# Kernel tuning notes

Hardware: AMD Instinct MI355X
Metric: run time of the kernel (lower is better)

The kernel has to match this reference:

```python
import jax, jax.numpy as jnp
import numpy as np

N_NODES = 50000
N_EDGES = 800000
IN_FEATS, H_FEATS, OUT_FEATS = 64, 128, 64
NUM_RELS = 2


def setup_inputs() -> dict:
    key = jax.random.key(0)
    ks = jax.random.split(key, 10)
    s = 0.05
    return {
        "feat": jax.random.normal(ks[0], (N_NODES, IN_FEATS), dtype=jnp.float32),
        "W1": jax.random.normal(ks[1], (NUM_RELS, IN_FEATS, H_FEATS), dtype=jnp.float32) * s,
        "loop1": jax.random.normal(ks[2], (IN_FEATS, H_FEATS), dtype=jnp.float32) * s,
        "b1": jnp.zeros((H_FEATS,), dtype=jnp.float32),
        "W2": jax.random.normal(ks[3], (NUM_RELS, H_FEATS, OUT_FEATS), dtype=jnp.float32) * s,
        "loop2": jax.random.normal(ks[4], (H_FEATS, OUT_FEATS), dtype=jnp.float32) * s,
        "b2": jnp.zeros((OUT_FEATS,), dtype=jnp.float32),
        "src": jax.random.randint(ks[5], (N_EDGES,), 0, N_NODES, dtype=jnp.int32),
        "dst": jax.random.randint(ks[6], (N_EDGES,), 0, N_NODES, dtype=jnp.int32),
        "etype": jax.random.randint(ks[7], (N_EDGES,), 0, NUM_RELS, dtype=jnp.int32),
    }


def _rel_graph_conv(x, W, loop_w, b, src, dst, etype, n_nodes):
    # Per-relation transform at node granularity (cheaper than per-edge W gather
    # since E >> N), then per-edge select by relation, gather by src,
    # scatter-sum into dst. Matches DGL RelGraphConv (regularizer=None,
    # self_loop=True, bias=True, sum aggregation).
    x0 = x @ W[0]  # [N, out]
    x1 = x @ W[1]  # [N, out]
    msg = jnp.where((etype == 0)[:, None], x0[src], x1[src])  # [E, out]
    agg = jax.ops.segment_sum(msg, dst, num_segments=n_nodes)  # [N, out]
    return agg + x @ loop_w + b


def reference(feat, W1, loop1, b1, W2, loop2, b2, src, dst, etype):
    n = feat.shape[0]
    h = _rel_graph_conv(feat, W1, loop1, b1, src, dst, etype, n)
    h = jax.nn.relu(h)
    h = _rel_graph_conv(h, W2, loop2, b2, src, dst, etype, n)
    return h
```

## Files before the change

kernel.cpp:

```cpp
#include <hip/hip_runtime.h>
#include <hip/hip_bf16.h>


#define N_IN   64
#define N_HID  128
#define N_OUT  64

typedef __attribute__((ext_vector_type(8))) short  bf16x8;
typedef __attribute__((ext_vector_type(4))) float  f32x4;

__device__ __forceinline__ ushort f2bf(float f) {
    uint u = __float_as_uint(f);
    u += 0x7FFFu + ((u >> 16) & 1u);
    return (ushort)(u >> 16);
}
__device__ __forceinline__ float bf2f(ushort h) {
    return __uint_as_float(((uint)h) << 16);
}
__device__ __forceinline__ float bfu_lo(uint u) { return __uint_as_float(u << 16); }
__device__ __forceinline__ float bfu_hi(uint u) { return __uint_as_float(u & 0xFFFF0000u); }

__global__ void hist_kernel(const int* __restrict__ dst, int* __restrict__ cnt, int E) {
    for (int e = blockIdx.x * blockDim.x + threadIdx.x; e < E;
         e += gridDim.x * blockDim.x)
        atomicAdd(&cnt[dst[e]], 1);
}

__global__ void scan_reduce_kernel(const int* __restrict__ cnt, int* __restrict__ bsum, int N) {
    __shared__ int s[1024];
    int i = blockIdx.x * 1024 + threadIdx.x;
    s[threadIdx.x] = (i < N) ? cnt[i] : 0;
    __syncthreads();
    for (int st = 512; st > 0; st >>= 1) {
        if ((int)threadIdx.x < st) s[threadIdx.x] += s[threadIdx.x + st];
        __syncthreads();
    }
    if (threadIdx.x == 0) bsum[blockIdx.x] = s[0];
}

__global__ void scan_top_kernel(const int* __restrict__ bsum, int* __restrict__ bx,
                                int NB, int* __restrict__ offN) {
    int l = threadIdx.x;
    int v = (l < NB) ? bsum[l] : 0;
    int x = v;
    for (int s = 1; s < 64; s <<= 1) {
        int t = __shfl_up(x, (unsigned)s, 64);
        if (l >= s) x += t;
    }
    if (l < NB) bx[l] = x - v;
    if (l == 63) *offN = x;
}

__global__ void scan_block_kernel(const int* __restrict__ cnt, const int* __restrict__ bx,
                                  int* __restrict__ off, int* __restrict__ cur, int N) {
    __shared__ int s[1024];
    int i = blockIdx.x * 1024 + threadIdx.x;
    int v = (i < N) ? cnt[i] : 0;
    s[threadIdx.x] = v;
    __syncthreads();
    for (int st = 1; st < 1024; st <<= 1) {
        int t = ((int)threadIdx.x >= st) ? s[threadIdx.x - st] : 0;
        __syncthreads();
        s[threadIdx.x] += t;
        __syncthreads();
    }
    if (i < N) {
        int e = bx[blockIdx.x] + s[threadIdx.x] - v;
        off[i] = e;
        cur[i] = e;
    }
}

__global__ void fill_kernel(const int* __restrict__ src, const int* __restrict__ dst,
                            const int* __restrict__ et, int* __restrict__ cur,
                            int* __restrict__ ent, int E) {
    for (int e = blockIdx.x * blockDim.x + threadIdx.x; e < E;
         e += gridDim.x * blockDim.x) {
        int pos = atomicAdd(&cur[dst[e]], 1);
        ent[pos] = (src[e] << 1) | et[e];
    }
}

__global__ void cvt_f32_bf16_kernel(const float* __restrict__ in,
                                    ushort* __restrict__ out, int n4) {
    for (int i = blockIdx.x * blockDim.x + threadIdx.x; i < n4;
         i += gridDim.x * blockDim.x) {
        float4 v = reinterpret_cast<const float4*>(in)[i];
        ushort4 o;
        o.x = f2bf(v.x); o.y = f2bf(v.y); o.z = f2bf(v.z); o.w = f2bf(v.w);
        reinterpret_cast<ushort4*>(out)[i] = o;
    }
}

template <int KTOT, int C>
__global__ void cvt_weights_kernel(const float* __restrict__ W,
                                   const float* __restrict__ loopw,
                                   ushort* __restrict__ dst) {
    const int TOT = 3 * C * KTOT;
    int q = blockIdx.x * blockDim.x + threadIdx.x;
    if (q >= TOT) return;
    int k = q / (3 * C), jgc = q % (3 * C);
    int sec = jgc / C, col = jgc % C;
    float v = (sec < 2) ? W[((size_t)sec * KTOT + k) * C + col]
                        : loopw[(size_t)k * C + col];
    int p = jgc >> 6, cin = jgc & 63;
    int di = p * (64 * KTOT) +
             (((cin >> 4) * (KTOT / 8) + (k >> 3)) * 16 + (cin & 15)) * 8 + (k & 7);
    dst[di] = f2bf(v);
}

template <int KTOT, int C>
__global__ __launch_bounds__(256, 4) void mfma_transform_kernel(
    const ushort* __restrict__ Xb,
    const ushort* __restrict__ Wf,
    const float*  __restrict__ bias,
    ushort* __restrict__ x0, ushort* __restrict__ x1, ushort* __restrict__ baseb,
    int M) {
    constexpr int CPR = KTOT / 8;
    constexpr int NKB = KTOT / 32;
    __shared__ ushort Al[128 * KTOT];

    const int row0 = blockIdx.x * 128;
    const int by   = blockIdx.y;
    const int sec  = (by * 64) / C;
    const int cof  = (by * 64) % C;

    const int wid  = threadIdx.x >> 6;
    const int wm   = wid >> 1, wn = wid & 1;
    const int lane = threadIdx.x & 63;

    const ushort* Wp = Wf + (size_t)by * (64 * KTOT);
    bf16x8 bfrag[2][NKB];
#pragma unroll
    for (int j = 0; j < 2; ++j)
#pragma unroll
        for (int kb = 0; kb < NKB; ++kb)
            bfrag[j][kb] = *reinterpret_cast<const bf16x8*>(
                Wp + ((wn * 2 + j) * CPR + kb * 4) * 128 + lane * 8);

    constexpr int CH = 128 * CPR;
    for (int ch = threadIdx.x; ch < CH; ch += 256) {
        int r = ch / CPR, kk8 = ch % CPR;
        int grow = row0 + r;
        uint4 v = make_uint4(0u, 0u, 0u, 0u);
        if (grow < M)
            v = *reinterpret_cast<const uint4*>(Xb + (size_t)grow * KTOT + kk8 * 8);
        int di = (((r >> 4) * CPR + kk8) * 16 + (r & 15)) * 8;
        *reinterpret_cast<uint4*>(&Al[di]) = v;
    }
    __syncthreads();

    f32x4 acc[4][2] = {};
#pragma unroll
    for (int kb = 0; kb < NKB; ++kb) {
        bf16x8 afrag[4];
#pragma unroll
        for (int i = 0; i < 4; ++i)
            afrag[i] = *reinterpret_cast<const bf16x8*>(
                &Al[((wm * 4 + i) * CPR + kb * 4) * 128 + lane * 8]);
#pragma unroll
        for (int i = 0; i < 4; ++i)
#pragma unroll
            for (int j = 0; j < 2; ++j)
                acc[i][j] = __builtin_amdgcn_mfma_f32_16x16x32_bf16(
                    afrag[i], bfrag[j][kb], acc[i][j], 0, 0, 0);
    }

    ushort* dst = (sec == 0) ? x0 : (sec == 1) ? x1 : baseb;
#pragma unroll
    for (int i = 0; i < 4; ++i) {
        int grow0 = row0 + (wm * 4 + i) * 16 + (lane >> 4) * 4;
#pragma unroll
        for (int j = 0; j < 2; ++j) {
            int scol = cof + wn * 32 + j * 16 + (lane & 15);
            float badd = (sec == 2) ? bias[scol] : 0.0f;
#pragma unroll
            for (int jj = 0; jj < 4; ++jj) {
                int grow = grow0 + jj;
                if (grow < M)
                    dst[(size_t)grow * C + scol] = f2bf(acc[i][j][jj] + badd);
            }
        }
    }
}

template <int C, bool RELU, bool OUTBF>
__global__ void gather_agg_kernel(const ushort* __restrict__ x0,
                                  const ushort* __restrict__ x1,
                                  const ushort* __restrict__ baseb,
                                  const int* __restrict__ off,
                                  const int* __restrict__ ent,
                                  ushort* __restrict__ outb,
                                  float* __restrict__ outf, int N) {
    constexpr int LPR = C / 8;
    constexpr int G   = 64 / LPR;
    int wid  = (int)((blockIdx.x * blockDim.x + threadIdx.x) >> 6);
    int lane = threadIdx.x & 63;
    if (wid >= N) return;
    const int g  = lane / LPR;
    const int li = lane % LPR;

    uint4 bv = make_uint4(0u, 0u, 0u, 0u);
    if (g == 0)
        bv = *reinterpret_cast<const uint4*>(baseb + (size_t)wid * C + li * 8);

    float acc[8];
#pragma unroll
    for (int k = 0; k < 8; ++k) acc[k] = 0.0f;

    const int e1 = off[wid + 1];
    int j = off[wid] + g;
    int p = (j < e1) ? ent[j] : -1;
    while (p >= 0) {
        int jn = j + G;
        int pn = (jn < e1) ? ent[jn] : -1;
        const ushort* row = ((p & 1) ? x1 : x0) + (size_t)(p >> 1) * C + li * 8;
        uint4 v = *reinterpret_cast<const uint4*>(row);
        acc[0] += bfu_lo(v.x); acc[1] += bfu_hi(v.x);
        acc[2] += bfu_lo(v.y); acc[3] += bfu_hi(v.y);
        acc[4] += bfu_lo(v.z); acc[5] += bfu_hi(v.z);
        acc[6] += bfu_lo(v.w); acc[7] += bfu_hi(v.w);
        p = pn; j = jn;
    }

#pragma unroll
    for (int m = LPR; m < 64; m <<= 1) {
#pragma unroll
        for (int k = 0; k < 8; ++k) acc[k] += __shfl_xor(acc[k], m, 64);
    }

    if (g == 0) {
        acc[0] += bfu_lo(bv.x); acc[1] += bfu_hi(bv.x);
        acc[2] += bfu_lo(bv.y); acc[3] += bfu_hi(bv.y);
        acc[4] += bfu_lo(bv.z); acc[5] += bfu_hi(bv.z);
        acc[6] += bfu_lo(bv.w); acc[7] += bfu_hi(bv.w);
        if (RELU) {
#pragma unroll
            for (int k = 0; k < 8; ++k) acc[k] = fmaxf(acc[k], 0.0f);
        }
        if (OUTBF) {
            uint4 o;
            o.x = (uint)f2bf(acc[0]) | ((uint)f2bf(acc[1]) << 16);
            o.y = (uint)f2bf(acc[2]) | ((uint)f2bf(acc[3]) << 16);
            o.z = (uint)f2bf(acc[4]) | ((uint)f2bf(acc[5]) << 16);
            o.w = (uint)f2bf(acc[6]) | ((uint)f2bf(acc[7]) << 16);
            *reinterpret_cast<uint4*>(outb + (size_t)wid * C + li * 8) = o;
        } else {
            float4 o0 = make_float4(acc[0], acc[1], acc[2], acc[3]);
            float4 o1 = make_float4(acc[4], acc[5], acc[6], acc[7]);
            float* dp = outf + (size_t)wid * C + li * 8;
            *reinterpret_cast<float4*>(dp)     = o0;
            *reinterpret_cast<float4*>(dp + 4) = o1;
        }
    }
}

extern "C" void kernel_launch(void* const* d_in, const int* in_sizes, int n_in,
                              void* d_out, int out_size, void* d_ws, size_t ws_size,
                              hipStream_t stream) {
    const float* feat  = (const float*)d_in[0];
    const float* W1    = (const float*)d_in[1];
    const float* loop1 = (const float*)d_in[2];
    const float* b1    = (const float*)d_in[3];
    const float* W2    = (const float*)d_in[4];
    const float* loop2 = (const float*)d_in[5];
    const float* b2    = (const float*)d_in[6];
    const int*   src   = (const int*)d_in[7];
    const int*   dst   = (const int*)d_in[8];
    const int*   et    = (const int*)d_in[9];
    float*       out   = (float*)d_out;

    const int N = in_sizes[0] / N_IN;
    const int E = in_sizes[7];

    char* wsb = (char*)d_ws;
    int* cnt  = (int*)wsb;
    int* off  = cnt + N;
    int* cur  = off + N + 1;
    int* bsum = cur + N;
    int* bx   = bsum + 64;
    int* ent  = bx + 64;
    size_t ibytes = (((size_t)(3 * N + 129 + E) * sizeof(int)) + 255) & ~(size_t)255;
    ushort* featb = (ushort*)(wsb + ibytes);
    ushort* hb    = featb + (size_t)N * N_IN;
    ushort* x0b   = hb    + (size_t)N * N_HID;
    ushort* x1b   = x0b   + (size_t)N * N_HID;
    ushort* baseb = x1b   + (size_t)N * N_HID;
    ushort* W1f   = baseb + (size_t)N * N_HID;
    ushort* W2f   = W1f + 3 * N_HID * N_IN;

    const int BLK  = 256;
    const int gE   = min((E + BLK - 1) / BLK, 2048);
    const int NB   = (N + 1023) / 1024;
    const int mT   = (N + 127) / 128;
    const int gAgg = (N * 64 + BLK - 1) / BLK;
    const int gCvF = min((N * N_IN / 4 + BLK - 1) / BLK, 2048);

    hipMemsetAsync(cnt, 0, (size_t)N * sizeof(int), stream);
    hist_kernel<<<gE, BLK, 0, stream>>>(dst, cnt, E);
    scan_reduce_kernel<<<NB, 1024, 0, stream>>>(cnt, bsum, N);
    scan_top_kernel<<<1, 64, 0, stream>>>(bsum, bx, NB, off + N);
    scan_block_kernel<<<NB, 1024, 0, stream>>>(cnt, bx, off, cur, N);
    fill_kernel<<<gE, BLK, 0, stream>>>(src, dst, et, cur, ent, E);

    cvt_f32_bf16_kernel<<<gCvF, BLK, 0, stream>>>(feat, featb, N * N_IN / 4);
    cvt_weights_kernel<N_IN, N_HID><<<(3 * N_HID * N_IN + BLK - 1) / BLK, BLK, 0, stream>>>(
        W1, loop1, W1f);
    cvt_weights_kernel<N_HID, N_OUT><<<(3 * N_OUT * N_HID + BLK - 1) / BLK, BLK, 0, stream>>>(
        W2, loop2, W2f);

    mfma_transform_kernel<N_IN, N_HID><<<dim3(mT, 3 * N_HID / 64), BLK, 0, stream>>>(
        featb, W1f, b1, x0b, x1b, baseb, N);
    gather_agg_kernel<N_HID, true, true><<<gAgg, BLK, 0, stream>>>(
        x0b, x1b, baseb, off, ent, hb, nullptr, N);

    mfma_transform_kernel<N_HID, N_OUT><<<dim3(mT, 3 * N_OUT / 64), BLK, 0, stream>>>(
        hb, W2f, b2, x0b, x1b, baseb, N);
    gather_agg_kernel<N_OUT, false, false><<<gAgg, BLK, 0, stream>>>(
        x0b, x1b, baseb, off, ent, nullptr, out, N);
}
```

Measured before the change: 280.9 us.

## Record per-edge rank in histogram and fuse feat conversion into transform

The histogram kernel now saves each edge's atomic return value as its rank within the destination bucket. The fill kernel then writes entries at off[dst]+rank with no second round of atomics, and the cur array disappears. Separately, the first-layer transform reads fp32 features directly and converts them to bf16 while staging into LDS, which removes the standalone conversion kernel and its intermediate buffer. The cost is an extra E-sized rank array to write and read, plus fp32 loads repeated across the six column blocks of the first transform.

```diff
diff --git a/kernel.cpp b/kernel.cpp
--- a/kernel.cpp
+++ b/kernel.cpp
@@ -20,10 +20,11 @@
 __device__ __forceinline__ float bfu_lo(uint u) { return __uint_as_float(u << 16); }
 __device__ __forceinline__ float bfu_hi(uint u) { return __uint_as_float(u & 0xFFFF0000u); }
 
-__global__ void hist_kernel(const int* __restrict__ dst, int* __restrict__ cnt, int E) {
+__global__ void hist_rank_kernel(const int* __restrict__ dst, int* __restrict__ cnt,
+                                 int* __restrict__ rank, int E) {
     for (int e = blockIdx.x * blockDim.x + threadIdx.x; e < E;
          e += gridDim.x * blockDim.x)
-        atomicAdd(&cnt[dst[e]], 1);
+        rank[e] = atomicAdd(&cnt[dst[e]], 1);
 }
 
 __global__ void scan_reduce_kernel(const int* __restrict__ cnt, int* __restrict__ bsum, int N) {
@@ -52,7 +53,7 @@
 }
 
 __global__ void scan_block_kernel(const int* __restrict__ cnt, const int* __restrict__ bx,
-                                  int* __restrict__ off, int* __restrict__ cur, int N) {
+                                  int* __restrict__ off, int N) {
     __shared__ int s[1024];
     int i = blockIdx.x * 1024 + threadIdx.x;
     int v = (i < N) ? cnt[i] : 0;
@@ -64,32 +65,15 @@
         s[threadIdx.x] += t;
         __syncthreads();
     }
-    if (i < N) {
-        int e = bx[blockIdx.x] + s[threadIdx.x] - v;
-        off[i] = e;
-        cur[i] = e;
-    }
+    if (i < N) off[i] = bx[blockIdx.x] + s[threadIdx.x] - v;
 }
 
 __global__ void fill_kernel(const int* __restrict__ src, const int* __restrict__ dst,
-                            const int* __restrict__ et, int* __restrict__ cur,
-                            int* __restrict__ ent, int E) {
+                            const int* __restrict__ et, const int* __restrict__ off,
+                            const int* __restrict__ rank, int* __restrict__ ent, int E) {
     for (int e = blockIdx.x * blockDim.x + threadIdx.x; e < E;
-         e += gridDim.x * blockDim.x) {
-        int pos = atomicAdd(&cur[dst[e]], 1);
-        ent[pos] = (src[e] << 1) | et[e];
-    }
-}
-
-__global__ void cvt_f32_bf16_kernel(const float* __restrict__ in,
-                                    ushort* __restrict__ out, int n4) {
-    for (int i = blockIdx.x * blockDim.x + threadIdx.x; i < n4;
-         i += gridDim.x * blockDim.x) {
-        float4 v = reinterpret_cast<const float4*>(in)[i];
-        ushort4 o;
-        o.x = f2bf(v.x); o.y = f2bf(v.y); o.z = f2bf(v.z); o.w = f2bf(v.w);
-        reinterpret_cast<ushort4*>(out)[i] = o;
-    }
+         e += gridDim.x * blockDim.x)
+        ent[off[dst[e]] + rank[e]] = (src[e] << 1) | et[e];
 }
 
 template <int KTOT, int C>
@@ -109,9 +93,9 @@
     dst[di] = f2bf(v);
 }
 
-template <int KTOT, int C>
+template <int KTOT, int C, bool INF32>
 __global__ __launch_bounds__(256, 4) void mfma_transform_kernel(
-    const ushort* __restrict__ Xb,
+    const void* __restrict__ Xsrc,
     const ushort* __restrict__ Wf,
     const float*  __restrict__ bias,
     ushort* __restrict__ x0, ushort* __restrict__ x1, ushort* __restrict__ baseb,
@@ -143,8 +127,20 @@
         int r = ch / CPR, kk8 = ch % CPR;
         int grow = row0 + r;
         uint4 v = make_uint4(0u, 0u, 0u, 0u);
-        if (grow < M)
-            v = *reinterpret_cast<const uint4*>(Xb + (size_t)grow * KTOT + kk8 * 8);
+        if (grow < M) {
+            if constexpr (INF32) {
+                const float* Xf = (const float*)Xsrc + (size_t)grow * KTOT + kk8 * 8;
+                float4 a = *reinterpret_cast<const float4*>(Xf);
+                float4 b = *reinterpret_cast<const float4*>(Xf + 4);
+                v.x = (uint)f2bf(a.x) | ((uint)f2bf(a.y) << 16);
+                v.y = (uint)f2bf(a.z) | ((uint)f2bf(a.w) << 16);
+                v.z = (uint)f2bf(b.x) | ((uint)f2bf(b.y) << 16);
+                v.w = (uint)f2bf(b.z) | ((uint)f2bf(b.w) << 16);
+            } else {
+                v = *reinterpret_cast<const uint4*>(
+                    (const ushort*)Xsrc + (size_t)grow * KTOT + kk8 * 8);
+            }
+        }
         int di = (((r >> 4) * CPR + kk8) * 16 + (r & 15)) * 8;
         *reinterpret_cast<uint4*>(&Al[di]) = v;
     }
@@ -276,13 +272,12 @@
     char* wsb = (char*)d_ws;
     int* cnt  = (int*)wsb;
     int* off  = cnt + N;
-    int* cur  = off + N + 1;
-    int* bsum = cur + N;
+    int* bsum = off + N + 1;
     int* bx   = bsum + 64;
-    int* ent  = bx + 64;
-    size_t ibytes = (((size_t)(3 * N + 129 + E) * sizeof(int)) + 255) & ~(size_t)255;
-    ushort* featb = (ushort*)(wsb + ibytes);
-    ushort* hb    = featb + (size_t)N * N_IN;
+    int* rank = bx + 64;
+    int* ent  = rank + E;
+    size_t ibytes = (((size_t)(2 * N + 129 + 2 * E) * sizeof(int)) + 255) & ~(size_t)255;
+    ushort* hb    = (ushort*)(wsb + ibytes);
     ushort* x0b   = hb    + (size_t)N * N_HID;
     ushort* x1b   = x0b   + (size_t)N * N_HID;
     ushort* baseb = x1b   + (size_t)N * N_HID;
@@ -294,27 +289,25 @@
     const int NB   = (N + 1023) / 1024;
     const int mT   = (N + 127) / 128;
     const int gAgg = (N * 64 + BLK - 1) / BLK;
-    const int gCvF = min((N * N_IN / 4 + BLK - 1) / BLK, 2048);
 
     hipMemsetAsync(cnt, 0, (size_t)N * sizeof(int), stream);
-    hist_kernel<<<gE, BLK, 0, stream>>>(dst, cnt, E);
+    hist_rank_kernel<<<gE, BLK, 0, stream>>>(dst, cnt, rank, E);
     scan_reduce_kernel<<<NB, 1024, 0, stream>>>(cnt, bsum, N);
     scan_top_kernel<<<1, 64, 0, stream>>>(bsum, bx, NB, off + N);
-    scan_block_kernel<<<NB, 1024, 0, stream>>>(cnt, bx, off, cur, N);
-    fill_kernel<<<gE, BLK, 0, stream>>>(src, dst, et, cur, ent, E);
-
-    cvt_f32_bf16_kernel<<<gCvF, BLK, 0, stream>>>(feat, featb, N * N_IN / 4);
+    scan_block_kernel<<<NB, 1024, 0, stream>>>(cnt, bx, off, N);
+    fill_kernel<<<gE, BLK, 0, stream>>>(src, dst, et, off, rank, ent, E);
+
     cvt_weights_kernel<N_IN, N_HID><<<(3 * N_HID * N_IN + BLK - 1) / BLK, BLK, 0, stream>>>(
         W1, loop1, W1f);
     cvt_weights_kernel<N_HID, N_OUT><<<(3 * N_OUT * N_HID + BLK - 1) / BLK, BLK, 0, stream>>>(
         W2, loop2, W2f);
 
-    mfma_transform_kernel<N_IN, N_HID><<<dim3(mT, 3 * N_HID / 64), BLK, 0, stream>>>(
-        featb, W1f, b1, x0b, x1b, baseb, N);
+    mfma_transform_kernel<N_IN, N_HID, true><<<dim3(mT, 3 * N_HID / 64), BLK, 0, stream>>>(
+        feat, W1f, b1, x0b, x1b, baseb, N);
     gather_agg_kernel<N_HID, true, true><<<gAgg, BLK, 0, stream>>>(
         x0b, x1b, baseb, off, ent, hb, nullptr, N);
 
-    mfma_transform_kernel<N_HID, N_OUT><<<dim3(mT, 3 * N_OUT / 64), BLK, 0, stream>>>(
+    mfma_transform_kernel<N_HID, N_OUT, false><<<dim3(mT, 3 * N_OUT / 64), BLK, 0, stream>>>(
         hb, W2f, b2, x0b, x1b, baseb, N);
     gather_agg_kernel<N_OUT, false, false><<<gAgg, BLK, 0, stream>>>(
         x0b, x1b, baseb, off, ent, nullptr, out, N);
```

After: 241.5 us. 14.0% less time.
